# Performance work log

Hardware: AMD Instinct MI355X
Metric: run time of the kernel (lower is better)

## Reference

```python
import jax, jax.numpy as jnp
import numpy as np

TAU = 2.0
V_TH = 1.0


def setup_inputs() -> dict:
    key = jax.random.key(0)
    k1, k2, k3 = jax.random.split(key, 3)
    T, B, H = 128, 64, 1024
    x = jax.random.normal(k1, (T, B, H), dtype=jnp.float32)
    # nn.Linear(H, H, bias=False) weights, shape [out, in]
    W1 = jax.random.normal(k2, (H, H), dtype=jnp.float32) / np.sqrt(H)
    W2 = jax.random.normal(k3, (H, H), dtype=jnp.float32) / np.sqrt(H)
    return {"x": x, "W1": W1, "W2": W2}


def _lif_scan(x_proj):
    # x_proj: [T, B, H]; membrane v starts at 0.
    def step(v, xt):
        h = v + (xt - v) / TAU          # leaky integrate
        s = (h >= V_TH).astype(h.dtype)  # hard-threshold spike
        v_new = h * (1.0 - s)            # soft reset (to 0 on spike)
        return v_new, s

    v0 = jnp.zeros(x_proj.shape[1:], dtype=x_proj.dtype)
    _, spikes = jax.lax.scan(step, v0, x_proj)
    return spikes  # [T, B, H]


def reference(x, W1, W2):
    # fc1 applied per timestep == one batched GEMM over [T*B, H]
    x_proj = jnp.einsum('tbh,oh->tbo', x, W1)
    spike = _lif_scan(x_proj)
    out = jnp.einsum('tbh,oh->tbo', spike, W2)
    return out
```

## Files before the change

### kernel.cpp

```cpp
#include <hip/hip_runtime.h>
#include <hip/hip_bf16.h>
#include <stdint.h>

#define TT 128
#define BB 64
#define HH 1024
#define MM (TT * BB)
#define NLANE (BB * HH)
#define DELTA 1.0e-4
#define F16_ONE 0x3C00

typedef __attribute__((ext_vector_type(8))) short bf16x8;
typedef __attribute__((ext_vector_type(8))) _Float16 f16x8;
typedef __attribute__((ext_vector_type(4))) float f32x4;

#define GLOAD16(g, l)                                                        \
    __builtin_amdgcn_global_load_lds(                                        \
        (const __attribute__((address_space(1))) unsigned int*)(g),          \
        (__attribute__((address_space(3))) unsigned int*)(l), 16, 0, 0)

#define FENCE() __builtin_amdgcn_sched_barrier(0)

static __device__ __forceinline__ unsigned short bf16_bits(float f) {
    __hip_bfloat16 b = __float2bfloat16(f);
    return *reinterpret_cast<unsigned short*>(&b);
}
static __device__ __forceinline__ unsigned short f16_bits(float f) {
    _Float16 h = (_Float16)f;
    return *reinterpret_cast<unsigned short*>(&h);
}

__global__ __launch_bounds__(256) void prep_fused(const float* __restrict__ x,
                                                  const float* __restrict__ W1,
                                                  const float* __restrict__ W2,
                                                  unsigned short* __restrict__ A2,
                                                  unsigned short* __restrict__ B2,
                                                  unsigned short* __restrict__ w2h,
                                                  int* __restrict__ cnt) {
    const int bid = blockIdx.x;
    if (bid == 0 && threadIdx.x == 0) *cnt = 0;

    if (bid < 9216) {
        const bool isX = (bid < 8192);
        const int i = (isX ? bid : bid - 8192) * 256 + threadIdx.x;
        const float4 v4 = reinterpret_cast<const float4*>(isX ? x : W1)[i];
        float v[4] = {v4.x, v4.y, v4.z, v4.w};
        unsigned short hb[4], lb[4];
#pragma unroll
        for (int c = 0; c < 4; c++) {
            hb[c] = bf16_bits(v[c]);
            __hip_bfloat16 hh = *reinterpret_cast<__hip_bfloat16*>(&hb[c]);
            lb[c] = bf16_bits(v[c] - __bfloat162float(hh));
        }
        ushort4* dst = reinterpret_cast<ushort4*>(isX ? A2 : B2);
        const int r = i >> 8;
        const int c4 = i & 255;
        dst[(size_t)r * 512 + c4]       = make_ushort4(hb[0], hb[1], hb[2], hb[3]);
        dst[(size_t)r * 512 + 256 + c4] = make_ushort4(lb[0], lb[1], lb[2], lb[3]);
    } else {
        const int i = (bid - 9216) * 256 + threadIdx.x;
        const float4 v4 = reinterpret_cast<const float4*>(W2)[i];
        float v[4] = {v4.x, v4.y, v4.z, v4.w};
        unsigned short hb[4];
#pragma unroll
        for (int c = 0; c < 4; c++) hb[c] = f16_bits(v[c]);
        reinterpret_cast<ushort4*>(w2h)[i] = make_ushort4(hb[0], hb[1], hb[2], hb[3]);
    }
}

__global__ __launch_bounds__(256, 1) void gemm1_w128(const unsigned short* __restrict__ A2,
                                                     const unsigned short* __restrict__ B2,
                                                     float* __restrict__ C) {
    __shared__ short As_[3][256 * 64];
    __shared__ short Bs_[3][128 * 64];

    const int tid = threadIdx.x;
    const int lane = tid & 63;
    const int wave = tid >> 6;
    const int wr = wave >> 1;
    const int wc = wave & 1;

    const int bid = blockIdx.x;
    const int orig = (bid & 7) * 32 + (bid >> 3);
    const int m0 = (orig >> 3) * 256;
    const int n0 = (orig & 7) * 128;

    const int rsel = lane & 15;
    const int part = lane >> 4;

    int adrA[8], adrB[4];
#pragma unroll
    for (int mi = 0; mi < 8; mi++) {
        const int ra = wr * 128 + mi * 16 + rsel;
        adrA[mi] = ra * 64 + ((part ^ (ra & 7)) << 3);
    }
#pragma unroll
    for (int ni = 0; ni < 4; ni++) {
        const int rb = wc * 64 + ni * 16 + rsel;
        adrB[ni] = rb * 64 + ((part ^ (rb & 7)) << 3);
    }

    const int srow = tid >> 3;
    const int lsw  = (tid & 7) ^ (srow & 7);
    const int src_sw = (lsw & 3) * 8 + (lsw >> 2) * 1024;
    const int ldso = wave * 512;

#define STAGE_A(buf, q, kc)                                                       \
    GLOAD16(&A2[(size_t)(m0 + (q) * 32 + srow) * 2048 + (kc) + src_sw],           \
            &As_[buf][(q) * 2048 + ldso])
#define STAGE_B(buf, b, kc)                                                       \
    GLOAD16(&B2[(size_t)(n0 + (b) * 32 + srow) * 2048 + (kc) + src_sw],           \
            &Bs_[buf][(b) * 2048 + ldso])
#define STAGE_G1(buf, kc)  do { STAGE_A(buf,0,kc); STAGE_A(buf,1,kc); STAGE_A(buf,2,kc); STAGE_A(buf,3,kc); } while (0)
#define STAGE_G2(buf, kc)  do { STAGE_A(buf,4,kc); STAGE_A(buf,5,kc); STAGE_A(buf,6,kc); STAGE_A(buf,7,kc); } while (0)
#define STAGE_G3(buf, kc)  do { STAGE_B(buf,0,kc); STAGE_B(buf,1,kc); STAGE_B(buf,2,kc); STAGE_B(buf,3,kc); } while (0)

    f32x4 acc[8][4] = {};

    STAGE_G1(0, 0); STAGE_G2(0, 0); STAGE_G3(0, 0);
    STAGE_G1(1, 32); STAGE_G2(1, 32); STAGE_G3(1, 32);
    asm volatile("s_waitcnt vmcnt(12)" ::: "memory");
    FENCE();
    __builtin_amdgcn_s_barrier();
    FENCE();

    int bufr = 0;

    for (int t = 0; t < 32; ++t) {
        const short* As = As_[bufr];
        const short* Bs = Bs_[bufr];
        const int bstg = (bufr + 2 >= 3) ? bufr - 1 : bufr + 2;
        const int tc = (t + 2 < 32) ? t + 2 : 31;
        const int kc2 = tc * 32;

        bf16x8 aH[8], aL[8], bH[4], bL[4];

        aH[0] = *reinterpret_cast<const bf16x8*>(&As[adrA[0]]);
#pragma unroll
        for (int ni = 0; ni < 4; ni++)
            bH[ni] = *reinterpret_cast<const bf16x8*>(&Bs[adrB[ni]]);
#pragma unroll
        for (int mi = 1; mi < 8; mi++)
            aH[mi] = *reinterpret_cast<const bf16x8*>(&As[adrA[mi]]);
        FENCE();
        STAGE_G1(bstg, kc2);
        FENCE();

#pragma unroll
        for (int mi = 0; mi < 8; mi++)
#pragma unroll
            for (int ni = 0; ni < 4; ni++)
                acc[mi][ni] = __builtin_amdgcn_mfma_f32_16x16x32_bf16(aH[mi], bH[ni], acc[mi][ni], 0, 0, 0);
        FENCE();

#pragma unroll
        for (int ni = 0; ni < 4; ni++)
            bL[ni] = *reinterpret_cast<const bf16x8*>(&Bs[adrB[ni] ^ 32]);
#pragma unroll
        for (int mi = 0; mi < 8; mi++)
            aL[mi] = *reinterpret_cast<const bf16x8*>(&As[adrA[mi] ^ 32]);
        FENCE();
        STAGE_G2(bstg, kc2);
        STAGE_G3(bstg, kc2);
        FENCE();

#pragma unroll
        for (int mi = 0; mi < 8; mi++)
#pragma unroll
            for (int ni = 0; ni < 4; ni++)
                acc[mi][ni] = __builtin_amdgcn_mfma_f32_16x16x32_bf16(aH[mi], bL[ni], acc[mi][ni], 0, 0, 0);
        FENCE();

#pragma unroll
        for (int mi = 0; mi < 8; mi++)
#pragma unroll
            for (int ni = 0; ni < 4; ni++)
                acc[mi][ni] = __builtin_amdgcn_mfma_f32_16x16x32_bf16(aL[mi], bH[ni], acc[mi][ni], 0, 0, 0);
        FENCE();

        asm volatile("s_waitcnt vmcnt(12) lgkmcnt(0)" ::: "memory");
        FENCE();
        __builtin_amdgcn_s_barrier();
        FENCE();

        bufr = (bufr == 2) ? 0 : bufr + 1;
    }
#undef STAGE_G1
#undef STAGE_G2
#undef STAGE_G3
#undef STAGE_A
#undef STAGE_B

    asm volatile("s_waitcnt vmcnt(0) lgkmcnt(0)" ::: "memory");
    FENCE();

    const int col = lane & 15;
    const int quad = lane >> 4;
#pragma unroll
    for (int mi = 0; mi < 8; mi++)
#pragma unroll
        for (int ni = 0; ni < 4; ni++) {
            const int m = m0 + wr * 128 + mi * 16 + quad * 4;
            const int n = n0 + wc * 64 + ni * 16 + col;
            float* dst = &C[(size_t)m * HH + n];
#pragma unroll
            for (int r = 0; r < 4; r++)
                dst[(size_t)r * HH] = acc[mi][ni][r];
        }
}

__global__ __launch_bounds__(256) void lif_scan_flag(const float* __restrict__ xp,
                                                     unsigned short* __restrict__ sp,
                                                     int* __restrict__ count,
                                                     int* __restrict__ list) {
    const int idx = blockIdx.x * 256 + threadIdx.x;
    double v = 0.0;
    bool flg = false;
#pragma unroll 4
    for (int t = 0; t < TT; t++) {
        const double x = (double)xp[(size_t)t * NLANE + idx];
        const double h = v + (x - v) * 0.5;
        const bool s = (h >= 1.0);
        flg |= (fabs(h - 1.0) < DELTA);
        v = s ? 0.0 : h;
        sp[(size_t)t * NLANE + idx] = s ? (unsigned short)F16_ONE : (unsigned short)0;
    }
    if (flg) {
        const int i = atomicAdd(count, 1);
        list[i] = idx;
    }
}

__global__ __launch_bounds__(1024) void recompute_fused(const float* __restrict__ X,
                                                        const float* __restrict__ W1,
                                                        const int* __restrict__ count,
                                                        const int* __restrict__ list,
                                                        unsigned short* __restrict__ sp) {
    __shared__ double hbuf[TT];
    const int cnt = *count;
    const int wv = threadIdx.x >> 6;
    const int ln = threadIdx.x & 63;

    for (int li = blockIdx.x; li < cnt; li += gridDim.x) {
        const int lane = list[li];
        const int b = lane >> 10;
        const int h = lane & (HH - 1);
        const float4* w4 = reinterpret_cast<const float4*>(W1 + (size_t)h * HH);

        for (int t = wv; t < TT; t += 16) {
            const float4* x4 = reinterpret_cast<const float4*>(X + (size_t)(t * BB + b) * HH);
            double s0 = 0.0, s1 = 0.0, s2 = 0.0, s3 = 0.0;
#pragma unroll
            for (int i = 0; i < 4; i++) {
                const float4 xa = x4[ln + i * 64];
                const float4 wa = w4[ln + i * 64];
                s0 = fma((double)xa.x, (double)wa.x, s0);
                s1 = fma((double)xa.y, (double)wa.y, s1);
                s2 = fma((double)xa.z, (double)wa.z, s2);
                s3 = fma((double)xa.w, (double)wa.w, s3);
            }
            double s = (s0 + s1) + (s2 + s3);
#pragma unroll
            for (int off = 32; off >= 1; off >>= 1)
                s += __shfl_down(s, off);
            if (ln == 0) hbuf[t] = s;
        }
        __syncthreads();

        if (threadIdx.x == 0) {
            double v = 0.0;
            for (int t = 0; t < TT; t++) {
                const double hh = v + (hbuf[t] - v) * 0.5;
                const bool s = (hh >= 1.0);
                v = s ? 0.0 : hh;
                sp[(size_t)t * NLANE + lane] = s ? (unsigned short)F16_ONE : (unsigned short)0;
            }
        }
        __syncthreads();
    }
}

__global__ __launch_bounds__(256) void gemm2_mfma(const unsigned short* __restrict__ S,
                                                  const unsigned short* __restrict__ W,
                                                  float* __restrict__ O) {
    __shared__ short As[128 * 32];
    __shared__ short Bs[64 * 32];

    const int tid = threadIdx.x;
    const int lane = tid & 63;
    const int wave = tid >> 6;
    const int m0 = blockIdx.y * 128;
    const int n0 = blockIdx.x * 64;
    const int wm = (wave >> 1) * 64;
    const int wn = (wave & 1) * 32;

    const int rsel = lane & 15;
    const int part = lane >> 4;

    int adrA[4], adrB[2];
#pragma unroll
    for (int i = 0; i < 4; i++) {
        const int ra = wm + i * 16 + rsel;
        adrA[i] = ra * 32 + (part ^ ((ra >> 1) & 3)) * 8;
    }
#pragma unroll
    for (int i = 0; i < 2; i++) {
        const int rb = wn + i * 16 + rsel;
        adrB[i] = rb * 32 + (part ^ ((rb >> 1) & 3)) * 8;
    }

    f32x4 acc[4][2] = {};

    for (int k0 = 0; k0 < HH; k0 += 32) {
#pragma unroll
        for (int p = 0; p < 3; p++) {
            const int c = tid + p * 256;
            const int cb = wave * 64 + p * 256;
            if (c < 512) {
                const int row = c >> 2;
                const int pslot = c & 3;
                const int pdata = pslot ^ ((row >> 1) & 3);
                GLOAD16(&S[(size_t)(m0 + row) * HH + k0 + pdata * 8], &As[cb * 8]);
            } else {
                const int c2 = c - 512;
                const int row = c2 >> 2;
                const int pslot = c2 & 3;
                const int pdata = pslot ^ ((row >> 1) & 3);
                GLOAD16(&W[(size_t)(n0 + row) * HH + k0 + pdata * 8], &Bs[(cb - 512) * 8]);
            }
        }
        __syncthreads();

        f16x8 a[4], b[2];
#pragma unroll
        for (int mi = 0; mi < 4; mi++)
            a[mi] = *reinterpret_cast<f16x8*>(&As[adrA[mi]]);
#pragma unroll
        for (int ni = 0; ni < 2; ni++)
            b[ni] = *reinterpret_cast<f16x8*>(&Bs[adrB[ni]]);

#pragma unroll
        for (int mi = 0; mi < 4; mi++)
#pragma unroll
            for (int ni = 0; ni < 2; ni++)
                acc[mi][ni] = __builtin_amdgcn_mfma_f32_16x16x32_f16(
                    a[mi], b[ni], acc[mi][ni], 0, 0, 0);

        __syncthreads();
    }

    const int col = lane & 15;
    const int quad = lane >> 4;
#pragma unroll
    for (int mi = 0; mi < 4; mi++)
#pragma unroll
        for (int ni = 0; ni < 2; ni++) {
            const int m = m0 + wm + mi * 16 + quad * 4;
            const int n = n0 + wn + ni * 16 + col;
            float* dst = &O[(size_t)m * HH + n];
#pragma unroll
            for (int r = 0; r < 4; r++)
                dst[(size_t)r * HH] = acc[mi][ni][r];
        }
}

extern "C" void kernel_launch(void* const* d_in, const int* in_sizes, int n_in,
                              void* d_out, int out_size, void* d_ws, size_t ws_size,
                              hipStream_t stream) {
    const float* x  = (const float*)d_in[0];
    const float* W1 = (const float*)d_in[1];
    const float* W2 = (const float*)d_in[2];
    float* out = (float*)d_out;

    char* ws = (char*)d_ws;

    unsigned short* A2   = (unsigned short*)ws;
    unsigned short* B2   = A2 + (size_t)MM * 2048;
    unsigned short* w2h  = B2 + (size_t)HH * 2048;
    int*            list = (int*)(w2h + (size_t)HH * HH);
    int*            cnt  = list + NLANE;
    float*          xp   = (float*)(((uintptr_t)(cnt + 64) + 255) & ~(uintptr_t)255);
    unsigned short* sp   = (unsigned short*)ws;

    prep_fused<<<10240, 256, 0, stream>>>(x, W1, W2, A2, B2, w2h, cnt);

    gemm1_w128<<<256, 256, 0, stream>>>(A2, B2, xp);

    lif_scan_flag<<<NLANE / 256, 256, 0, stream>>>(xp, sp, cnt, list);

    recompute_fused<<<512, 1024, 0, stream>>>(x, W1, cnt, list, sp);

    dim3 g2(HH / 64, MM / 128);
    gemm2_mfma<<<g2, 256, 0, stream>>>(sp, w2h, out);
}
```

Measured before the change: 221.1 us.

## Shrink gemm1 tile to 128x128 with double buffering for two blocks per CU

Replaces the 256x128-tile, triple-buffered split-bf16 GEMM1 with a 128x128 tile and two LDS buffers, so two blocks can share a CU and the grid grows from 256 to 512 blocks. The prefetch of the next k-slice is issued at the top of each iteration, and the MFMA loop is wrapped in s_setprio. This aims to improve occupancy and load balance across CUs. In exchange it reduces per-block operand reuse, since each A/B byte feeds fewer MFMAs. It also makes each iteration wait for all outstanding loads (vmcnt(0)), which cuts pipelining depth.

```diff
diff --git a/kernel.cpp b/kernel.cpp
--- a/kernel.cpp
+++ b/kernel.cpp
@@ -68,11 +68,11 @@
     }
 }
 
-__global__ __launch_bounds__(256, 1) void gemm1_w128(const unsigned short* __restrict__ A2,
-                                                     const unsigned short* __restrict__ B2,
-                                                     float* __restrict__ C) {
-    __shared__ short As_[3][256 * 64];
-    __shared__ short Bs_[3][128 * 64];
+__global__ __launch_bounds__(256, 2) void gemm1_db(const unsigned short* __restrict__ A2,
+                                                   const unsigned short* __restrict__ B2,
+                                                   float* __restrict__ C) {
+    __shared__ short As_[2][128 * 64];
+    __shared__ short Bs_[2][128 * 64];
 
     const int tid = threadIdx.x;
     const int lane = tid & 63;
@@ -81,17 +81,17 @@
     const int wc = wave & 1;
 
     const int bid = blockIdx.x;
-    const int orig = (bid & 7) * 32 + (bid >> 3);
-    const int m0 = (orig >> 3) * 256;
+    const int orig = (bid & 7) * 64 + (bid >> 3);
+    const int m0 = (orig >> 3) * 128;
     const int n0 = (orig & 7) * 128;
 
     const int rsel = lane & 15;
     const int part = lane >> 4;
 
-    int adrA[8], adrB[4];
-#pragma unroll
-    for (int mi = 0; mi < 8; mi++) {
-        const int ra = wr * 128 + mi * 16 + rsel;
+    int adrA[4], adrB[4];
+#pragma unroll
+    for (int mi = 0; mi < 4; mi++) {
+        const int ra = wr * 64 + mi * 16 + rsel;
         adrA[mi] = ra * 64 + ((part ^ (ra & 7)) << 3);
     }
 #pragma unroll
@@ -111,96 +111,70 @@
 #define STAGE_B(buf, b, kc)                                                       \
     GLOAD16(&B2[(size_t)(n0 + (b) * 32 + srow) * 2048 + (kc) + src_sw],           \
             &Bs_[buf][(b) * 2048 + ldso])
-#define STAGE_G1(buf, kc)  do { STAGE_A(buf,0,kc); STAGE_A(buf,1,kc); STAGE_A(buf,2,kc); STAGE_A(buf,3,kc); } while (0)
-#define STAGE_G2(buf, kc)  do { STAGE_A(buf,4,kc); STAGE_A(buf,5,kc); STAGE_A(buf,6,kc); STAGE_A(buf,7,kc); } while (0)
-#define STAGE_G3(buf, kc)  do { STAGE_B(buf,0,kc); STAGE_B(buf,1,kc); STAGE_B(buf,2,kc); STAGE_B(buf,3,kc); } while (0)
-
-    f32x4 acc[8][4] = {};
-
-    STAGE_G1(0, 0); STAGE_G2(0, 0); STAGE_G3(0, 0);
-    STAGE_G1(1, 32); STAGE_G2(1, 32); STAGE_G3(1, 32);
-    asm volatile("s_waitcnt vmcnt(12)" ::: "memory");
+#define STAGE8(buf, kc)                                                           \
+    do {                                                                          \
+        STAGE_A(buf, 0, kc); STAGE_A(buf, 1, kc);                                 \
+        STAGE_A(buf, 2, kc); STAGE_A(buf, 3, kc);                                 \
+        STAGE_B(buf, 0, kc); STAGE_B(buf, 1, kc);                                 \
+        STAGE_B(buf, 2, kc); STAGE_B(buf, 3, kc);                                 \
+    } while (0)
+
+    f32x4 acc[4][4] = {};
+
+    STAGE8(0, 0);
+    asm volatile("s_waitcnt vmcnt(0)" ::: "memory");
     FENCE();
     __builtin_amdgcn_s_barrier();
     FENCE();
 
-    int bufr = 0;
-
     for (int t = 0; t < 32; ++t) {
-        const short* As = As_[bufr];
-        const short* Bs = Bs_[bufr];
-        const int bstg = (bufr + 2 >= 3) ? bufr - 1 : bufr + 2;
-        const int tc = (t + 2 < 32) ? t + 2 : 31;
-        const int kc2 = tc * 32;
-
-        bf16x8 aH[8], aL[8], bH[4], bL[4];
-
-        aH[0] = *reinterpret_cast<const bf16x8*>(&As[adrA[0]]);
-#pragma unroll
-        for (int ni = 0; ni < 4; ni++)
+        const int buf = t & 1;
+        const short* As = As_[buf];
+        const short* Bs = Bs_[buf];
+        const int tn = (t + 1 < 32) ? t + 1 : 31;
+
+        STAGE8(buf ^ 1, tn * 32);
+        FENCE();
+
+        bf16x8 aH[4], aL[4], bH[4], bL[4];
+#pragma unroll
+        for (int mi = 0; mi < 4; mi++) {
+            aH[mi] = *reinterpret_cast<const bf16x8*>(&As[adrA[mi]]);
+            aL[mi] = *reinterpret_cast<const bf16x8*>(&As[adrA[mi] ^ 32]);
+        }
+#pragma unroll
+        for (int ni = 0; ni < 4; ni++) {
             bH[ni] = *reinterpret_cast<const bf16x8*>(&Bs[adrB[ni]]);
-#pragma unroll
-        for (int mi = 1; mi < 8; mi++)
-            aH[mi] = *reinterpret_cast<const bf16x8*>(&As[adrA[mi]]);
-        FENCE();
-        STAGE_G1(bstg, kc2);
-        FENCE();
-
-#pragma unroll
-        for (int mi = 0; mi < 8; mi++)
-#pragma unroll
-            for (int ni = 0; ni < 4; ni++)
+            bL[ni] = *reinterpret_cast<const bf16x8*>(&Bs[adrB[ni] ^ 32]);
+        }
+
+        __builtin_amdgcn_s_setprio(1);
+#pragma unroll
+        for (int mi = 0; mi < 4; mi++)
+#pragma unroll
+            for (int ni = 0; ni < 4; ni++) {
                 acc[mi][ni] = __builtin_amdgcn_mfma_f32_16x16x32_bf16(aH[mi], bH[ni], acc[mi][ni], 0, 0, 0);
-        FENCE();
-
-#pragma unroll
-        for (int ni = 0; ni < 4; ni++)
-            bL[ni] = *reinterpret_cast<const bf16x8*>(&Bs[adrB[ni] ^ 32]);
-#pragma unroll
-        for (int mi = 0; mi < 8; mi++)
-            aL[mi] = *reinterpret_cast<const bf16x8*>(&As[adrA[mi] ^ 32]);
-        FENCE();
-        STAGE_G2(bstg, kc2);
-        STAGE_G3(bstg, kc2);
-        FENCE();
-
-#pragma unroll
-        for (int mi = 0; mi < 8; mi++)
-#pragma unroll
-            for (int ni = 0; ni < 4; ni++)
                 acc[mi][ni] = __builtin_amdgcn_mfma_f32_16x16x32_bf16(aH[mi], bL[ni], acc[mi][ni], 0, 0, 0);
-        FENCE();
-
-#pragma unroll
-        for (int mi = 0; mi < 8; mi++)
-#pragma unroll
-            for (int ni = 0; ni < 4; ni++)
                 acc[mi][ni] = __builtin_amdgcn_mfma_f32_16x16x32_bf16(aL[mi], bH[ni], acc[mi][ni], 0, 0, 0);
-        FENCE();
-
-        asm volatile("s_waitcnt vmcnt(12) lgkmcnt(0)" ::: "memory");
+            }
+        __builtin_amdgcn_s_setprio(0);
+
+        asm volatile("s_waitcnt vmcnt(0) lgkmcnt(0)" ::: "memory");
         FENCE();
         __builtin_amdgcn_s_barrier();
         FENCE();
-
-        bufr = (bufr == 2) ? 0 : bufr + 1;
-    }
-#undef STAGE_G1
-#undef STAGE_G2
-#undef STAGE_G3
+    }
+#undef STAGE8
 #undef STAGE_A
 #undef STAGE_B
 
-    asm volatile("s_waitcnt vmcnt(0) lgkmcnt(0)" ::: "memory");
-    FENCE();
-
     const int col = lane & 15;
     const int quad = lane >> 4;
 #pragma unroll
-    for (int mi = 0; mi < 8; mi++)
+    for (int mi = 0; mi < 4; mi++)
 #pragma unroll
         for (int ni = 0; ni < 4; ni++) {
-            const int m = m0 + wr * 128 + mi * 16 + quad * 4;
+            const int m = m0 + wr * 64 + mi * 16 + quad * 4;
             const int n = n0 + wc * 64 + ni * 16 + col;
             float* dst = &C[(size_t)m * HH + n];
 #pragma unroll
@@ -384,7 +358,7 @@
 
     prep_fused<<<10240, 256, 0, stream>>>(x, W1, W2, A2, B2, w2h, cnt);
 
-    gemm1_w128<<<256, 256, 0, stream>>>(A2, B2, xp);
+    gemm1_db<<<512, 256, 0, stream>>>(A2, B2, xp);
 
     lif_scan_flag<<<NLANE / 256, 256, 0, stream>>>(xp, sp, cnt, list);
 
```

After: 212.0 us. 1.04x faster.
